# Kernel tuning notes

Measured on AMD Instinct MI355X. Metric: run time of the kernel, lower is better.

Reference implementation:

```python
import jax, jax.numpy as jnp
import numpy as np

L, M, K = 13, 12, 5
ODD_KS = tuple(range(1, K + 1, 2))  # (1, 3, 5) -> n_odd_order = 3
NK = len(ODD_KS)


def setup_inputs() -> dict:
    key = jax.random.key(0)
    k1, k2, k3, k4 = jax.random.split(key, 4)
    B, T = 16, 8192
    x = jax.random.normal(k1, (B, T, 2), dtype=jnp.float32)
    h_0 = jnp.zeros((B, 16), dtype=jnp.float32)  # unused by forward (API compat)
    A_kl = jax.random.normal(k2, (L, NK), dtype=jnp.float32) * 0.1
    B_klm = jax.random.normal(k3, (L, M, NK), dtype=jnp.float32) * 0.1
    C_klm = jax.random.normal(k4, (L, M, NK), dtype=jnp.float32) * 0.1
    return {"x": x, "h_0": h_0, "A_kl": A_kl, "B_klm": B_klm, "C_klm": C_klm}


def _gmp_forward(x, A_kl, B_klm, C_klm):
    # x: [B, T, 2] real/imag -> complex signal
    Bsz, T, _ = x.shape
    xc = jax.lax.complex(x[..., 0], x[..., 1])  # [B, T]

    # Circular window indices (equivalent to torch cat+unfold in the original).
    t = jnp.arange(T)[:, None, None]
    l = jnp.arange(L)[None, :, None]
    m = jnp.arange(M + 1)[None, None, :]
    # 2nd term pads with the LAST (L+M-1) samples at the front -> index shift back
    idx2 = (t + l + m - (L + M - 1)) % T  # [T, L, M+1]
    # 3rd term pads with the FIRST (L+M-1) samples at the end -> forward wrap
    idx3 = (t + l + m) % T                # [T, L, M+1]

    x2 = xc[:, idx2]  # [B, T, L, M+1] complex
    x3 = xc[:, idx3]  # [B, T, L, M+1] complex
    # First-term window x[t-(L-1)+l] equals the m=M element of the 2nd-term window.
    x1 = x2[..., -1]  # [B, T, L]

    # --- term 1: sum_{l,k} A[l,k] * x1 * |x1|^k ---
    a1 = jnp.abs(x1)                                        # [B,T,L]
    p1 = jnp.stack([a1 ** k for k in ODD_KS], axis=-1)       # [B,T,L,NK] real
    c1 = jnp.einsum('btlk,lk->btl', p1, A_kl)                # real coefficient
    term1 = jnp.sum(x1 * c1, axis=-1)                        # [B,T] complex

    # --- term 2: sum_{l,m,k} B[l,m,k] * x2[...,M] * |x2[...,m]|^k ---
    a2 = jnp.abs(x2[..., :-1])                               # [B,T,L,M]
    p2 = jnp.stack([a2 ** k for k in ODD_KS], axis=-1)       # [B,T,L,M,NK]
    c2 = jnp.einsum('btlmk,lmk->btl', p2, B_klm)             # sum over m,k too
    term2 = jnp.sum(x1 * c2, axis=-1)                        # multiplier is x2[...,-1]==x1

    # --- term 3: same structure with forward-lag windows and C ---
    x3_last = x3[..., -1]                                    # [B,T,L]
    a3 = jnp.abs(x3[..., :-1])                               # [B,T,L,M]
    p3 = jnp.stack([a3 ** k for k in ODD_KS], axis=-1)       # [B,T,L,M,NK]
    c3 = jnp.einsum('btlmk,lmk->btl', p3, C_klm)
    term3 = jnp.sum(x3_last * c3, axis=-1)

    s = term1 + term2 + term3                                # [B,T] complex
    return jnp.stack([jnp.real(s), jnp.imag(s)], axis=-1)    # [B,T,2] float32


def reference(x, h_0, A_kl, B_klm, C_klm):
    # h_0 is accepted but unused, matching the torch module.
    return _gmp_forward(x, A_kl, B_klm, C_klm)
```

## Files before the change

### kernel.cpp

```cpp
#include <hip/hip_runtime.h>
#include <math.h>

#define LL   13
#define MM   12
#define NKK  3
#define BLOCK 256
#define HALO  24
#define WIN  (BLOCK + 2*HALO)


__global__ __launch_bounds__(BLOCK)
void gmp_kernel(const float* __restrict__ x,
                const float* __restrict__ Ac,
                const float* __restrict__ Bc,
                const float* __restrict__ Cc,
                float* __restrict__ out,
                int T, int tilesPerB)
{
    __shared__ float4 sP[WIN];
    __shared__ float2 sZ[WIN];

    const int tid = threadIdx.x;
    const int b   = blockIdx.x / tilesPerB;
    const int t0  = (blockIdx.x % tilesPerB) * BLOCK;

    const float* xb = x + (size_t)b * T * 2;

    for (int j = tid; j < WIN; j += BLOCK) {
        int t = t0 - HALO + j;
        if (t < 0)  t += T;
        if (t >= T) t -= T;
        const float2 z = *(const float2*)(xb + 2 * t);
        float a2 = z.x * z.x + z.y * z.y;
        float a  = sqrtf(a2);
        sZ[j] = z;
        sP[j] = make_float4(a, a * a2, a * a2 * a2, 0.0f);
    }
    __syncthreads();

    float cB[LL], cC[LL];
    #pragma unroll
    for (int l = 0; l < LL; ++l) {
        const float4 p = sP[tid + l + 12];
        cB[l] = Ac[l * NKK + 0] * p.x
              + Ac[l * NKK + 1] * p.y
              + Ac[l * NKK + 2] * p.z;
        cC[l] = 0.0f;
    }

    #pragma unroll
    for (int d = 0; d < LL + MM - 1; ++d) {
        const float4 p = sP[tid + d];
        const float4 q = sP[tid + d + HALO];
        #pragma unroll
        for (int l = 0; l < LL; ++l) {
            const int m = d - l;
            if (m >= 0 && m < MM) {
                const float* bp = Bc + (l * MM + m) * NKK;
                cB[l] += bp[0] * p.x + bp[1] * p.y + bp[2] * p.z;
                const float* cp = Cc + (l * MM + m) * NKK;
                cC[l] += cp[0] * q.x + cp[1] * q.y + cp[2] * q.z;
            }
        }
    }

    float sr = 0.0f, si = 0.0f;
    #pragma unroll
    for (int l = 0; l < LL; ++l) {
        const float2 z1 = sZ[tid + l + 12];
        const float2 z3 = sZ[tid + l + 36];
        sr += z1.x * cB[l] + z3.x * cC[l];
        si += z1.y * cB[l] + z3.y * cC[l];
    }

    const int t = t0 + tid;
    if (t < T) {
        float2* op = (float2*)(out + ((size_t)b * T + t) * 2);
        *op = make_float2(sr, si);
    }
}

extern "C" void kernel_launch(void* const* d_in, const int* in_sizes, int n_in,
                              void* d_out, int out_size, void* d_ws, size_t ws_size,
                              hipStream_t stream)
{
    const float* x  = (const float*)d_in[0];
    const float* Ac = (const float*)d_in[2];
    const float* Bc = (const float*)d_in[3];
    const float* Cc = (const float*)d_in[4];
    float* out = (float*)d_out;

    const int Bsz = in_sizes[1] / 16;
    const int T   = in_sizes[0] / (2 * Bsz);
    const int tilesPerB = (T + BLOCK - 1) / BLOCK;

    dim3 grid(Bsz * tilesPerB);
    dim3 block(BLOCK);
    gmp_kernel<<<grid, block, 0, stream>>>(x, Ac, Bc, Cc, out, T, tilesPerB);
}
```

Baseline: 73.25 us.

## Compute two adjacent outputs per thread to share window loads

Each thread now produces two consecutive time outputs, so one shared-memory power load per lag serves both outputs through a sliding register pair, and the A-term is folded into the main lag loop. The block tile doubles to 512 samples, halving the grid, and outputs are written as a single float4 store. This roughly halves LDS traffic and the uniform coefficient loads per output, at the cost of about twice as many accumulator registers and fewer blocks in flight. The store guard now requires an even T.

```diff
diff --git a/kernel.cpp b/kernel.cpp
--- a/kernel.cpp
+++ b/kernel.cpp
@@ -1,12 +1,14 @@
 #include <hip/hip_runtime.h>
 #include <math.h>
 
-#define LL   13
-#define MM   12
-#define NKK  3
+#define LL    13
+#define MM    12
+#define NKK   3
 #define BLOCK 256
+#define RPT   2
+#define TILE  (BLOCK * RPT)
 #define HALO  24
-#define WIN  (BLOCK + 2*HALO)
+#define WIN   (TILE + 2 * HALO)
 
 
 __global__ __launch_bounds__(BLOCK)
@@ -21,8 +23,9 @@
     __shared__ float2 sZ[WIN];
 
     const int tid = threadIdx.x;
+    const int i0  = 2 * tid;
     const int b   = blockIdx.x / tilesPerB;
-    const int t0  = (blockIdx.x % tilesPerB) * BLOCK;
+    const int t0  = (blockIdx.x % tilesPerB) * TILE;
 
     const float* xb = x + (size_t)b * T * 2;
 
@@ -38,45 +41,65 @@
     }
     __syncthreads();
 
-    float cB[LL], cC[LL];
+    float cB0[LL], cC0[LL], cB1[LL], cC1[LL];
     #pragma unroll
-    for (int l = 0; l < LL; ++l) {
-        const float4 p = sP[tid + l + 12];
-        cB[l] = Ac[l * NKK + 0] * p.x
-              + Ac[l * NKK + 1] * p.y
-              + Ac[l * NKK + 2] * p.z;
-        cC[l] = 0.0f;
-    }
+    for (int l = 0; l < LL; ++l) { cB0[l] = cC0[l] = cB1[l] = cC1[l] = 0.0f; }
+
+    float4 pA = sP[i0];
+    float4 qA = sP[i0 + HALO];
 
     #pragma unroll
     for (int d = 0; d < LL + MM - 1; ++d) {
-        const float4 p = sP[tid + d];
-        const float4 q = sP[tid + d + HALO];
+        const float4 pB = sP[i0 + d + 1];
+        const float4 qB = sP[i0 + d + HALO + 1];
+
+        if (d == 0) {
+            const float* ap = Ac + 12 * NKK;
+            cB0[12] += ap[0] * qA.x + ap[1] * qA.y + ap[2] * qA.z;
+            cB1[12] += ap[0] * qB.x + ap[1] * qB.y + ap[2] * qB.z;
+        }
+        if (d >= 12) {
+            const int l = d - 12;
+            const float* ap = Ac + l * NKK;
+            cB0[l] += ap[0] * pA.x + ap[1] * pA.y + ap[2] * pA.z;
+            cB1[l] += ap[0] * pB.x + ap[1] * pB.y + ap[2] * pB.z;
+        }
+
         #pragma unroll
         for (int l = 0; l < LL; ++l) {
             const int m = d - l;
             if (m >= 0 && m < MM) {
                 const float* bp = Bc + (l * MM + m) * NKK;
-                cB[l] += bp[0] * p.x + bp[1] * p.y + bp[2] * p.z;
+                cB0[l] += bp[0] * pA.x + bp[1] * pA.y + bp[2] * pA.z;
+                cB1[l] += bp[0] * pB.x + bp[1] * pB.y + bp[2] * pB.z;
                 const float* cp = Cc + (l * MM + m) * NKK;
-                cC[l] += cp[0] * q.x + cp[1] * q.y + cp[2] * q.z;
+                cC0[l] += cp[0] * qA.x + cp[1] * qA.y + cp[2] * qA.z;
+                cC1[l] += cp[0] * qB.x + cp[1] * qB.y + cp[2] * qB.z;
             }
         }
+        pA = pB;
+        qA = qB;
     }
 
-    float sr = 0.0f, si = 0.0f;
+    float sr0 = 0.f, si0 = 0.f, sr1 = 0.f, si1 = 0.f;
+    float2 z1A = sZ[i0 + 12];
+    float2 z3A = sZ[i0 + 36];
     #pragma unroll
     for (int l = 0; l < LL; ++l) {
-        const float2 z1 = sZ[tid + l + 12];
-        const float2 z3 = sZ[tid + l + 36];
-        sr += z1.x * cB[l] + z3.x * cC[l];
-        si += z1.y * cB[l] + z3.y * cC[l];
+        const float2 z1B = sZ[i0 + l + 13];
+        const float2 z3B = sZ[i0 + l + 37];
+        sr0 += z1A.x * cB0[l] + z3A.x * cC0[l];
+        si0 += z1A.y * cB0[l] + z3A.y * cC0[l];
+        sr1 += z1B.x * cB1[l] + z3B.x * cC1[l];
+        si1 += z1B.y * cB1[l] + z3B.y * cC1[l];
+        z1A = z1B;
+        z3A = z3B;
     }
 
-    const int t = t0 + tid;
-    if (t < T) {
-        float2* op = (float2*)(out + ((size_t)b * T + t) * 2);
-        *op = make_float2(sr, si);
+    const int t = t0 + i0;
+    if (t + 1 < T) {
+        float4* op = (float4*)(out + ((size_t)b * T + t) * 2);
+        *op = make_float4(sr0, si0, sr1, si1);
     }
 }
 
@@ -92,7 +115,7 @@
 
     const int Bsz = in_sizes[1] / 16;
     const int T   = in_sizes[0] / (2 * Bsz);
-    const int tilesPerB = (T + BLOCK - 1) / BLOCK;
+    const int tilesPerB = (T + TILE - 1) / TILE;
 
     dim3 grid(Bsz * tilesPerB);
     dim3 block(BLOCK);
```

Measured after the change: 78.01 us. +6.5%, slower.
